# Performance work log

Hardware: AMD Instinct MI355X
Metric: run time of the kernel (lower is better)

## Reference

```python
import jax, jax.numpy as jnp
import numpy as np
import math

N = 10000      # num nodes
DEG = 3        # base avg out-degree of random directed graph
D = 128        # d_model
H = 8          # heads
C = D // H     # head dim
L = 2          # num_layers
HOPS = 2       # num_hops


def _build_attn_window(rng):
    # random directed base graph
    E0 = N * DEG
    s0 = rng.integers(0, N, E0).astype(np.int64)
    d0 = rng.integers(0, N, E0).astype(np.int64)
    # to_undirected + coalesce
    s = np.concatenate([s0, d0]); d = np.concatenate([d0, s0])
    key = np.unique(s * N + d)
    s, d = key // N, key % N
    # add self loops (as in _get_attn_window) and coalesce
    loops = np.arange(N, dtype=np.int64)
    key = np.unique(np.concatenate([loops * N + loops, s * N + d]))
    s, d = key // N, key % N
    # base adjacency in CSR-like form grouped by source
    order = np.argsort(s, kind='stable')
    bss, bsd = s[order], d[order]
    outdeg = np.bincount(bss, minlength=N)
    indptr = np.concatenate([[0], np.cumsum(outdeg)])
    # k_hop = A; for _ in range(HOPS-1): k_hop = k_hop @ A   (boolean sparse product)
    cs, cd = s.copy(), d.copy()
    for _ in range(HOPS - 1):
        counts = outdeg[cd]
        total = int(counts.sum())
        new_s = np.repeat(cs, counts)
        starts = np.repeat(indptr[cd], counts)
        offs = np.arange(total, dtype=np.int64) - np.repeat(
            np.concatenate([[0], np.cumsum(counts)])[:-1], counts)
        new_d = bsd[starts + offs]
        key = np.unique(new_s * N + new_d)
        cs, cd = key // N, key % N
    return np.stack([cs, cd]).astype(np.int64)  # [2, E2] (src, dst)


def setup_inputs() -> dict:
    rng = np.random.default_rng(0)
    aw = _build_attn_window(rng)
    key = jax.random.key(0)
    ks = jax.random.split(key, 10)
    sc = 1.0 / math.sqrt(D)
    x = jax.random.normal(ks[0], (N, D), jnp.float32)
    Wq = jax.random.normal(ks[1], (L, D, D), jnp.float32) * sc
    Wk = jax.random.normal(ks[2], (L, D, D), jnp.float32) * sc
    Wv = jax.random.normal(ks[3], (L, D, D), jnp.float32) * sc
    Ws = jax.random.normal(ks[4], (L, D, D), jnp.float32) * sc
    bq = jax.random.normal(ks[5], (L, D), jnp.float32) * 0.01
    bk = jax.random.normal(ks[6], (L, D), jnp.float32) * 0.01
    bv = jax.random.normal(ks[7], (L, D), jnp.float32) * 0.01
    bs = jax.random.normal(ks[8], (L, D), jnp.float32) * 0.01
    return {"x": x, "Wq": Wq, "bq": bq, "Wk": Wk, "bk": bk,
            "Wv": Wv, "bv": bv, "Ws": Ws, "bs": bs,
            "attn_window": jnp.asarray(aw)}


def _segment_softmax(logits, seg):
    # logits: [E, H], seg: [E] destination node ids (every node has a self loop)
    m = jax.ops.segment_max(logits, seg, num_segments=N)
    e = jnp.exp(logits - m[seg])
    z = jax.ops.segment_sum(e, seg, num_segments=N)
    return e / z[seg]


def _transformer_conv(h, wq, bq_, wk, bk_, wv, bv_, ws, bs_, src, dst):
    # PyG TransformerConv (concat=True, root_weight=True, beta=False, eval mode)
    q = (h @ wq + bq_).reshape(N, H, C)
    k = (h @ wk + bk_).reshape(N, H, C)
    v = (h @ wv + bv_).reshape(N, H, C)
    logits = jnp.einsum('ehc,ehc->eh', q[dst], k[src]) * (1.0 / math.sqrt(C))
    alpha = _segment_softmax(logits, dst)                       # [E, H]
    agg = jax.ops.segment_sum(alpha[:, :, None] * v[src], dst,  # [N, H, C]
                              num_segments=N)
    return agg.reshape(N, D) + h @ ws + bs_


def reference(x, Wq, bq, Wk, bk, Wv, bv, Ws, bs, attn_window):
    src, dst = attn_window[0], attn_window[1]
    h = x
    for l in range(L - 1):
        h = jax.nn.relu(h + _transformer_conv(
            h, Wq[l], bq[l], Wk[l], bk[l], Wv[l], bv[l], Ws[l], bs[l], src, dst))
    l = L - 1
    h = h + _transformer_conv(
        h, Wq[l], bq[l], Wk[l], bk[l], Wv[l], bv[l], Ws[l], bs[l], src, dst)
    return h
```

## Files before the change

kernel.cpp:

```cpp
#include <hip/hip_runtime.h>
#include <hip/hip_bf16.h>

typedef __hip_bfloat16 bf16;
typedef __attribute__((ext_vector_type(8))) short bf16x8v;
typedef __attribute__((ext_vector_type(4))) float f32x4v;
typedef __attribute__((ext_vector_type(2))) float f32x2v;

#define N_NODES 10000
#define DMODEL  128
#define NHEADS  8
#define CHEAD   16


#ifndef __has_builtin
#define __has_builtin(x) 0
#endif
#if __has_builtin(__builtin_amdgcn_cvt_pk_f32_fp8) && \
    __has_builtin(__builtin_amdgcn_cvt_pk_fp8_f32)
#define FP8_HW 1
#else
#define FP8_HW 0
#endif

__device__ __forceinline__ float bf2f(unsigned u) {
    union { unsigned i; float f; } c; c.i = u << 16; return c.f;
}
__device__ __forceinline__ unsigned short f2bf_bits(float f) {
    bf16 b = __float2bfloat16(f);
    return *(unsigned short*)&b;
}

__device__ __forceinline__ unsigned char f2fp8(float f) {
#if FP8_HW
    int p = __builtin_amdgcn_cvt_pk_fp8_f32(f, f, 0, false);
    return (unsigned char)(p & 0xff);
#else
    _Float16 hf = (_Float16)f;
    unsigned short u = *reinterpret_cast<unsigned short*>(&hf);
    unsigned s = (u >> 8) & 0x80u;
    unsigned mag = u & 0x7fffu;
    unsigned t = mag + 0x3Fu + ((mag >> 7) & 1u);
    int v = (int)(t >> 7) - 0x40;
    if (v < 0) v = 0;
    if (v > 0x7e) v = 0x7e;
    return (unsigned char)(s | (unsigned)v);
#endif
}
__device__ __forceinline__ void fp8x4_to_f32(unsigned w, float* f) {
#if FP8_HW
    f32x2v lo = __builtin_amdgcn_cvt_pk_f32_fp8((int)w, false);
    f32x2v hi = __builtin_amdgcn_cvt_pk_f32_fp8((int)w, true);
    f[0] = lo[0]; f[1] = lo[1]; f[2] = hi[0]; f[3] = hi[1];
#else
    #pragma unroll
    for (int i = 0; i < 4; ++i) {
        unsigned b = (w >> (8 * i)) & 0xffu;
        unsigned h = ((b & 0x80u) << 8) | (((b & 0x7fu) << 7) + 0x2000u);
        h = (b & 0x7fu) ? h : ((b & 0x80u) << 8);
        unsigned short us = (unsigned short)h;
        _Float16 f16 = *reinterpret_cast<_Float16*>(&us);
        f[i] = (float)f16;
    }
#endif
}

__global__ __launch_bounds__(256) void gemm_qkvs(
    const void* __restrict__ Ain, int a_is_bf16,
    const float* __restrict__ Wq, const float* __restrict__ Wk,
    const float* __restrict__ Wv, const float* __restrict__ Ws,
    const float* __restrict__ bq, const float* __restrict__ bk,
    const float* __restrict__ bv, const float* __restrict__ bs,
    int welem, int belem,
    float* __restrict__ qo, unsigned char* __restrict__ ko,
    bf16* __restrict__ vo, float* __restrict__ hso,
    const int* __restrict__ aw, int E,
    int* __restrict__ rowptr, int* __restrict__ nbr)
{
    __shared__ unsigned short As[64][136];
    __shared__ unsigned short Bs[128][68];
    __shared__ int nz;

    const int tid = threadIdx.x;

    if (E > 0) {
        if (tid == 0) nz = 0;
        __syncthreads();
        int W = 4096;
        if (W > 2 * E) W = 2 * E;
        int any = 0;
        for (int w = 1 + 2 * tid; w < W; w += 2 * (int)blockDim.x)
            any |= aw[w];
        if (any) atomicOr(&nz, 1);
        __syncthreads();
        const int is64 = (nz == 0);

        const int gid = (blockIdx.y * gridDim.x + blockIdx.x) * blockDim.x
                      + tid;
        const int gtot = gridDim.x * gridDim.y * blockDim.x;
        if (gid == 0) rowptr[N_NODES] = E;
        for (int e = gid; e < E; e += gtot) {
            int s  = is64 ? aw[2 * e] : aw[e];
            if (s < 0) s = 0;
            if (s >= N_NODES) s = N_NODES - 1;
            int sp = (e == 0) ? -1 : (is64 ? aw[2 * (e - 1)] : aw[e - 1]);
            for (int r = sp + 1; r <= s; ++r) rowptr[r] = e;
            if (e == E - 1)
                for (int r = s + 1; r < N_NODES; ++r) rowptr[r] = E;
            int d = is64 ? aw[2 * (E + e)] : aw[E + e];
            if (d < 0) d = 0;
            if (d >= N_NODES) d = N_NODES - 1;
            nbr[e] = d;
        }
        __syncthreads();
    }

    const int cb    = blockIdx.x;
    const int row0  = blockIdx.y * 64;
    const int mat   = cb >> 1;
    const float* W    = (mat == 0) ? Wq : (mat == 1) ? Wk
                      : (mat == 2) ? Wv : Ws;
    const float* bias = (mat == 0) ? bq : (mat == 1) ? bk
                      : (mat == 2) ? bv : bs;
    const int colW0 = (cb & 1) * 64;

    if (a_is_bf16) {
        const unsigned short* A = (const unsigned short*)Ain;
        #pragma unroll
        for (int i = 0; i < 4; ++i) {
            int idx = tid + i * 256;
            int row = idx >> 4, k8 = idx & 15;
            int grow = row0 + row;
            uint4 u = make_uint4(0u, 0u, 0u, 0u);
            if (grow < N_NODES)
                u = *(const uint4*)&A[grow * DMODEL + k8 * 8];
            *(uint4*)&As[row][k8 * 8] = u;
        }
    } else {
        const float* A = (const float*)Ain;
        #pragma unroll
        for (int i = 0; i < 8; ++i) {
            int idx = tid + i * 256;
            int row = idx >> 5, k4 = idx & 31;
            int grow = row0 + row;
            float4 av = make_float4(0.f, 0.f, 0.f, 0.f);
            if (grow < N_NODES)
                av = *(const float4*)&A[grow * DMODEL + k4 * 4];
            ushort4 p;
            p.x = f2bf_bits(av.x); p.y = f2bf_bits(av.y);
            p.z = f2bf_bits(av.z); p.w = f2bf_bits(av.w);
            *(ushort4*)&As[row][k4 * 4] = p;
        }
    }
    #pragma unroll
    for (int i = 0; i < 8; ++i) {
        int idx = tid + i * 256;
        int kk = idx >> 4, n4 = idx & 15;
        float4 wv = *(const float4*)&W[welem + kk * DMODEL + colW0 + n4 * 4];
        ushort4 p;
        p.x = f2bf_bits(wv.x); p.y = f2bf_bits(wv.y);
        p.z = f2bf_bits(wv.z); p.w = f2bf_bits(wv.w);
        *(ushort4*)&Bs[kk][n4 * 4] = p;
    }
    __syncthreads();

    const int wave = tid >> 6, lane = tid & 63;
    const int ln = lane & 15, quad = lane >> 4;
    const int ncol = wave * 16 + ln;

    f32x4v acc[4];
    #pragma unroll
    for (int mt = 0; mt < 4; ++mt) acc[mt] = (f32x4v){0.f, 0.f, 0.f, 0.f};

    #pragma unroll
    for (int ks = 0; ks < 4; ++ks) {
        const int kb = ks * 32 + quad * 8;
        bf16x8v bfv;
        #pragma unroll
        for (int j = 0; j < 8; ++j) bfv[j] = (short)Bs[kb + j][ncol];
        #pragma unroll
        for (int mt = 0; mt < 4; ++mt) {
            bf16x8v afv = *(const bf16x8v*)&As[mt * 16 + ln][kb];
            acc[mt] = __builtin_amdgcn_mfma_f32_16x16x32_bf16(
                afv, bfv, acc[mt], 0, 0, 0);
        }
    }

    const float bcol = bias[belem + colW0 + ncol];
    #pragma unroll
    for (int mt = 0; mt < 4; ++mt) {
        #pragma unroll
        for (int r = 0; r < 4; ++r) {
            int row = row0 + mt * 16 + quad * 4 + r;
            if (row >= N_NODES) continue;
            float val = acc[mt][r] + bcol;
            int elo = row * DMODEL + colW0 + ncol;
            if (mat == 0)      qo[elo] = val;
            else if (mat == 3) hso[elo] = val;
            else if (mat == 1) ko[elo] = f2fp8(val);
            else               vo[elo] = __float2bfloat16(val);
        }
    }
}

__global__ __launch_bounds__(256) void attn_fused(
    const float* __restrict__ q, const unsigned char* __restrict__ k,
    const bf16* __restrict__ v, const float* __restrict__ hs,
    const float* __restrict__ hin_f,
    const unsigned short* __restrict__ hin_b,
    const int* __restrict__ rowptr, const int* __restrict__ nbr,
    float* __restrict__ out, unsigned short* __restrict__ outb,
    int relu_flag)
{
    const int wid = blockIdx.x * 4 + (threadIdx.x >> 6);
    const int nWaves = gridDim.x * 4;
    const int l = threadIdx.x & 63;
    const int h = l & 7, slot = l >> 3;
    const int hc = l >> 3;

    for (int d = wid; d < N_NODES; d += nWaves) {
        float qf[16];
        const float* qp = q + d * DMODEL + h * CHEAD;
        #pragma unroll
        for (int i = 0; i < 4; ++i) {
            float4 t4 = *(const float4*)(qp + i * 4);
            qf[i * 4 + 0] = t4.x; qf[i * 4 + 1] = t4.y;
            qf[i * 4 + 2] = t4.z; qf[i * 4 + 3] = t4.w;
        }

        const int e0 = rowptr[d], e1 = rowptr[d + 1];
        float zacc = 0.f;
        float2 acc = make_float2(0.f, 0.f);

        int eg = e0 + slot;
        bool pad_cur = !(eg < e1);
        int s_cur = pad_cur ? d : nbr[eg];
        uint4 kc = *(const uint4*)(k + s_cur * DMODEL + h * CHEAD);

        for (int base = e0; base < e1; base += 8) {
            int en = base + 8 + slot;
            bool pad_nxt = !(en < e1);
            int s_nxt = pad_nxt ? d : nbr[en];
            uint4 kn = *(const uint4*)(k + s_nxt * DMODEL + h * CHEAD);

            int se[8];
            #pragma unroll
            for (int e = 0; e < 8; ++e) se[e] = __shfl(s_cur, e * 8);
            unsigned uv[8];
            #pragma unroll
            for (int e = 0; e < 8; ++e)
                uv[e] = *(const unsigned*)(v + se[e] * DMODEL + 2 * l);

            const unsigned* kw = (const unsigned*)&kc;
            float dot = 0.f;
            #pragma unroll
            for (int w = 0; w < 4; ++w) {
                float kf[4];
                fp8x4_to_f32(kw[w], kf);
                dot += qf[w * 4 + 0] * kf[0];
                dot += qf[w * 4 + 1] * kf[1];
                dot += qf[w * 4 + 2] * kf[2];
                dot += qf[w * 4 + 3] * kf[3];
            }
            float p = pad_cur ? -3.0e38f : fminf(dot * 0.25f, 60.f);
            float pe = __expf(p);
            zacc += pe;

            float pee[8];
            #pragma unroll
            for (int e = 0; e < 8; ++e) pee[e] = __shfl(pe, e * 8 + hc);
            #pragma unroll
            for (int e = 0; e < 8; ++e) {
                acc.x += pee[e] * bf2f(uv[e] & 0xffffu);
                acc.y += pee[e] * bf2f(uv[e] >> 16);
            }

            kc = kn; s_cur = s_nxt; pad_cur = pad_nxt;
        }

        float z = zacc;
        z += __shfl_xor(z, 8);
        z += __shfl_xor(z, 16);
        z += __shfl_xor(z, 32);
        float zh = __shfl(z, hc);
        float inv = (zh > 0.f) ? (1.f / zh) : 0.f;

        int idx = d * DMODEL + 2 * l;
        float2 hsv = *(const float2*)(hs + idx);
        float2 hiv;
        if (hin_f) {
            hiv = *(const float2*)(hin_f + idx);
        } else {
            unsigned u = *(const unsigned*)(hin_b + idx);
            hiv.x = bf2f(u & 0xffffu);
            hiv.y = bf2f(u >> 16);
        }
        float2 o;
        o.x = acc.x * inv + hsv.x + hiv.x;
        o.y = acc.y * inv + hsv.y + hiv.y;
        if (relu_flag) { o.x = fmaxf(o.x, 0.f); o.y = fmaxf(o.y, 0.f); }
        if (out) *(float2*)(out + idx) = o;
        if (outb) {
            unsigned pk = f2bf_bits(o.x) | ((unsigned)f2bf_bits(o.y) << 16);
            *(unsigned*)&outb[idx] = pk;
        }
    }
}

extern "C" void kernel_launch(void* const* d_in, const int* in_sizes, int n_in,
                              void* d_out, int out_size, void* d_ws, size_t ws_size,
                              hipStream_t stream) {
    const float* x  = (const float*)d_in[0];
    const float* Wq = (const float*)d_in[1];
    const float* bq = (const float*)d_in[2];
    const float* Wk = (const float*)d_in[3];
    const float* bk = (const float*)d_in[4];
    const float* Wv = (const float*)d_in[5];
    const float* bv = (const float*)d_in[6];
    const float* Ws = (const float*)d_in[7];
    const float* bs = (const float*)d_in[8];
    const int*   aw = (const int*)d_in[9];
    const int E = in_sizes[9] / 2;

    char* ws = (char*)d_ws;
    size_t off = 0;
    float* qb = (float*)(ws + off);  off += (size_t)N_NODES * DMODEL * 4;
    unsigned char* kb = (unsigned char*)(ws + off);
    off += (size_t)N_NODES * DMODEL;
    off = (off + 255) & ~(size_t)255;
    bf16*  vb = (bf16*)(ws + off);   off += (size_t)N_NODES * DMODEL * 2;
    float* hsb = (float*)(ws + off); off += (size_t)N_NODES * DMODEL * 4;
    unsigned short* h1b = (unsigned short*)(ws + off);
    off += (size_t)N_NODES * DMODEL * 2;
    int* rowptr = (int*)(ws + off);  off += ((size_t)N_NODES + 2) * 4;
    int* nbr    = (int*)(ws + off);  off += (size_t)E * 4;

    dim3 ggrid(8, (N_NODES + 63) / 64);
    const int ablocks = (N_NODES + 3) / 4;

    gemm_qkvs<<<ggrid, 256, 0, stream>>>(x, 0, Wq, Wk, Wv, Ws,
                                         bq, bk, bv, bs, 0, 0,
                                         qb, kb, vb, hsb, aw, E, rowptr, nbr);
    attn_fused<<<ablocks, 256, 0, stream>>>(qb, kb, vb, hsb, x,
                                            (const unsigned short*)0,
                                            rowptr, nbr,
                                            (float*)0, h1b, 1);
    gemm_qkvs<<<ggrid, 256, 0, stream>>>(h1b, 1, Wq, Wk, Wv, Ws,
                                         bq, bk, bv, bs,
                                         DMODEL * DMODEL, DMODEL,
                                         qb, kb, vb, hsb, aw, 0, rowptr, nbr);
    attn_fused<<<ablocks, 256, 0, stream>>>(qb, kb, vb, hsb,
                                            (const float*)0, h1b,
                                            rowptr, nbr,
                                            (float*)d_out,
                                            (unsigned short*)0, 0);
}
```

Measured before the change: 158.8 us.

## Split each node's edge list across two waves with LDS reduction

The attention kernel now runs one 128-thread block per destination node instead of one wave per node. The two waves take alternating groups of 8 edges, halving the serial per-node loop length, and then combine their partial numerators and softmax denominators through shared memory after a barrier. This shortens the latency-bound dependent gather chain per node and exposes more parallelism. In exchange it adds a block barrier, an LDS exchange, a duplicated q load in both waves, and more blocks to launch.

```diff
diff --git a/kernel.cpp b/kernel.cpp
--- a/kernel.cpp
+++ b/kernel.cpp
@@ -202,7 +202,7 @@
     }
 }
 
-__global__ __launch_bounds__(256) void attn_fused(
+__global__ __launch_bounds__(128) void attn_fused(
     const float* __restrict__ q, const unsigned char* __restrict__ k,
     const bf16* __restrict__ v, const float* __restrict__ hs,
     const float* __restrict__ hin_f,
@@ -211,79 +211,93 @@
     float* __restrict__ out, unsigned short* __restrict__ outb,
     int relu_flag)
 {
-    const int wid = blockIdx.x * 4 + (threadIdx.x >> 6);
-    const int nWaves = gridDim.x * 4;
+    __shared__ float lacc[2][64][2];
+    __shared__ float lz[2][64];
+
+    const int wv = threadIdx.x >> 6;
     const int l = threadIdx.x & 63;
     const int h = l & 7, slot = l >> 3;
     const int hc = l >> 3;
 
-    for (int d = wid; d < N_NODES; d += nWaves) {
-        float qf[16];
-        const float* qp = q + d * DMODEL + h * CHEAD;
-        #pragma unroll
-        for (int i = 0; i < 4; ++i) {
-            float4 t4 = *(const float4*)(qp + i * 4);
-            qf[i * 4 + 0] = t4.x; qf[i * 4 + 1] = t4.y;
-            qf[i * 4 + 2] = t4.z; qf[i * 4 + 3] = t4.w;
-        }
-
-        const int e0 = rowptr[d], e1 = rowptr[d + 1];
-        float zacc = 0.f;
-        float2 acc = make_float2(0.f, 0.f);
-
-        int eg = e0 + slot;
-        bool pad_cur = !(eg < e1);
-        int s_cur = pad_cur ? d : nbr[eg];
-        uint4 kc = *(const uint4*)(k + s_cur * DMODEL + h * CHEAD);
-
-        for (int base = e0; base < e1; base += 8) {
-            int en = base + 8 + slot;
-            bool pad_nxt = !(en < e1);
-            int s_nxt = pad_nxt ? d : nbr[en];
-            uint4 kn = *(const uint4*)(k + s_nxt * DMODEL + h * CHEAD);
-
-            int se[8];
-            #pragma unroll
-            for (int e = 0; e < 8; ++e) se[e] = __shfl(s_cur, e * 8);
-            unsigned uv[8];
-            #pragma unroll
-            for (int e = 0; e < 8; ++e)
-                uv[e] = *(const unsigned*)(v + se[e] * DMODEL + 2 * l);
-
-            const unsigned* kw = (const unsigned*)&kc;
-            float dot = 0.f;
-            #pragma unroll
-            for (int w = 0; w < 4; ++w) {
-                float kf[4];
-                fp8x4_to_f32(kw[w], kf);
-                dot += qf[w * 4 + 0] * kf[0];
-                dot += qf[w * 4 + 1] * kf[1];
-                dot += qf[w * 4 + 2] * kf[2];
-                dot += qf[w * 4 + 3] * kf[3];
-            }
-            float p = pad_cur ? -3.0e38f : fminf(dot * 0.25f, 60.f);
-            float pe = __expf(p);
-            zacc += pe;
-
-            float pee[8];
-            #pragma unroll
-            for (int e = 0; e < 8; ++e) pee[e] = __shfl(pe, e * 8 + hc);
-            #pragma unroll
-            for (int e = 0; e < 8; ++e) {
-                acc.x += pee[e] * bf2f(uv[e] & 0xffffu);
-                acc.y += pee[e] * bf2f(uv[e] >> 16);
-            }
-
-            kc = kn; s_cur = s_nxt; pad_cur = pad_nxt;
-        }
-
-        float z = zacc;
-        z += __shfl_xor(z, 8);
-        z += __shfl_xor(z, 16);
-        z += __shfl_xor(z, 32);
-        float zh = __shfl(z, hc);
-        float inv = (zh > 0.f) ? (1.f / zh) : 0.f;
-
+    const int d = blockIdx.x;
+
+    float qf[16];
+    const float* qp = q + d * DMODEL + h * CHEAD;
+    #pragma unroll
+    for (int i = 0; i < 4; ++i) {
+        float4 t4 = *(const float4*)(qp + i * 4);
+        qf[i * 4 + 0] = t4.x; qf[i * 4 + 1] = t4.y;
+        qf[i * 4 + 2] = t4.z; qf[i * 4 + 3] = t4.w;
+    }
+
+    const int e0 = rowptr[d], e1 = rowptr[d + 1];
+    float zacc = 0.f;
+    float2 acc = make_float2(0.f, 0.f);
+
+    const int start = e0 + wv * 8;
+    int eg = start + slot;
+    bool pad_cur = !(eg < e1);
+    int s_cur = pad_cur ? d : nbr[eg];
+    uint4 kc = *(const uint4*)(k + s_cur * DMODEL + h * CHEAD);
+
+    for (int base = start; base < e1; base += 16) {
+        int en = base + 16 + slot;
+        bool pad_nxt = !(en < e1);
+        int s_nxt = pad_nxt ? d : nbr[en];
+        uint4 kn = *(const uint4*)(k + s_nxt * DMODEL + h * CHEAD);
+
+        int se[8];
+        #pragma unroll
+        for (int e = 0; e < 8; ++e) se[e] = __shfl(s_cur, e * 8);
+        unsigned uv[8];
+        #pragma unroll
+        for (int e = 0; e < 8; ++e)
+            uv[e] = *(const unsigned*)(v + se[e] * DMODEL + 2 * l);
+
+        const unsigned* kw = (const unsigned*)&kc;
+        float dot = 0.f;
+        #pragma unroll
+        for (int w = 0; w < 4; ++w) {
+            float kf[4];
+            fp8x4_to_f32(kw[w], kf);
+            dot += qf[w * 4 + 0] * kf[0];
+            dot += qf[w * 4 + 1] * kf[1];
+            dot += qf[w * 4 + 2] * kf[2];
+            dot += qf[w * 4 + 3] * kf[3];
+        }
+        float p = pad_cur ? -3.0e38f : fminf(dot * 0.25f, 60.f);
+        float pe = __expf(p);
+        zacc += pe;
+
+        float pee[8];
+        #pragma unroll
+        for (int e = 0; e < 8; ++e) pee[e] = __shfl(pe, e * 8 + hc);
+        #pragma unroll
+        for (int e = 0; e < 8; ++e) {
+            acc.x += pee[e] * bf2f(uv[e] & 0xffffu);
+            acc.y += pee[e] * bf2f(uv[e] >> 16);
+        }
+
+        kc = kn; s_cur = s_nxt; pad_cur = pad_nxt;
+    }
+
+    lacc[wv][l][0] = acc.x; lacc[wv][l][1] = acc.y; lz[wv][l] = zacc;
+    __syncthreads();
+    const int ow = wv ^ 1;
+    acc.x += lacc[ow][l][0];
+    acc.y += lacc[ow][l][1];
+    zacc  += lz[ow][l];
+
+    float z = zacc;
+    z += __shfl_xor(z, 8);
+    z += __shfl_xor(z, 16);
+    z += __shfl_xor(z, 32);
+    float zh = __shfl(z, hc);
+    float inv = (zh > 0.f) ? (1.f / zh) : 0.f;
+
+    const bool do_f32 = (out  != 0) && (wv == 0);
+    const bool do_bf  = (outb != 0) && (wv == 1);
+    if (do_f32 || do_bf) {
         int idx = d * DMODEL + 2 * l;
         float2 hsv = *(const float2*)(hs + idx);
         float2 hiv;
@@ -298,8 +312,8 @@
         o.x = acc.x * inv + hsv.x + hiv.x;
         o.y = acc.y * inv + hsv.y + hiv.y;
         if (relu_flag) { o.x = fmaxf(o.x, 0.f); o.y = fmaxf(o.y, 0.f); }
-        if (out) *(float2*)(out + idx) = o;
-        if (outb) {
+        if (do_f32) *(float2*)(out + idx) = o;
+        if (do_bf) {
             unsigned pk = f2bf_bits(o.x) | ((unsigned)f2bf_bits(o.y) << 16);
             *(unsigned*)&outb[idx] = pk;
         }
@@ -335,12 +349,11 @@
     int* nbr    = (int*)(ws + off);  off += (size_t)E * 4;
 
     dim3 ggrid(8, (N_NODES + 63) / 64);
-    const int ablocks = (N_NODES + 3) / 4;
 
     gemm_qkvs<<<ggrid, 256, 0, stream>>>(x, 0, Wq, Wk, Wv, Ws,
                                          bq, bk, bv, bs, 0, 0,
                                          qb, kb, vb, hsb, aw, E, rowptr, nbr);
-    attn_fused<<<ablocks, 256, 0, stream>>>(qb, kb, vb, hsb, x,
+    attn_fused<<<N_NODES, 128, 0, stream>>>(qb, kb, vb, hsb, x,
                                             (const unsigned short*)0,
                                             rowptr, nbr,
                                             (float*)0, h1b, 1);
@@ -348,7 +361,7 @@
                                          bq, bk, bv, bs,
                                          DMODEL * DMODEL, DMODEL,
                                          qb, kb, vb, hsb, aw, 0, rowptr, nbr);
-    attn_fused<<<ablocks, 256, 0, stream>>>(qb, kb, vb, hsb,
+    attn_fused<<<N_NODES, 128, 0, stream>>>(qb, kb, vb, hsb,
                                             (const float*)0, h1b,
                                             rowptr, nbr,
                                             (float*)d_out,
```

Result: faster. 154.6 us (-2.6%).
